# Performance work log

Hardware: AMD Instinct MI355X
Metric: run time of the kernel (lower is better)

Reference implementation:

```python
import jax, jax.numpy as jnp
import numpy as np

E, H, M = 1024, 16, 256
B, S = 2, 2048
D = E // H
SCALE = D ** -0.5


def setup_inputs() -> dict:
    key = jax.random.key(0)
    ks = jax.random.split(key, 10)
    p = 0.02
    return {
        "x": jax.random.normal(ks[0], (B, S, E), jnp.float32),
        "Wq": jax.random.normal(ks[1], (E, E), jnp.float32) * p,
        "bq": jax.random.normal(ks[2], (E,), jnp.float32) * p,
        "Wk": jax.random.normal(ks[3], (E, E), jnp.float32) * p,
        "bk": jax.random.normal(ks[4], (E,), jnp.float32) * p,
        "Wv": jax.random.normal(ks[5], (E, E), jnp.float32) * p,
        "bv": jax.random.normal(ks[6], (E,), jnp.float32) * p,
        "Wo": jax.random.normal(ks[7], (E, E), jnp.float32) * p,
        "bo": jax.random.normal(ks[8], (E,), jnp.float32) * p,
        "memory_state": jax.random.normal(ks[9], (M, E), jnp.float32) * p,
    }


def reference(x, Wq, bq, Wk, bk, Wv, bv, Wo, bo, memory_state):
    b, s, e = x.shape
    # QKV projections (torch Linear: y = x W^T + b), split heads -> [b,h,s,d]
    q = (x @ Wq.T + bq).reshape(b, s, H, D).transpose(0, 2, 1, 3)
    k = (x @ Wk.T + bk).reshape(b, s, H, D).transpose(0, 2, 1, 3)
    v = (x @ Wv.T + bv).reshape(b, s, H, D).transpose(0, 2, 1, 3)
    # full self-attention (eval mode: dropout is identity)
    attn = jax.nn.softmax(jnp.einsum("bhqd,bhkd->bhqk", q, k) * SCALE, axis=-1)
    attn_out = jnp.einsum("bhqk,bhkd->bhqd", attn, v)
    attn_out = attn_out.transpose(0, 2, 1, 3).reshape(b, s, e)
    # memory-read cross-attention on raw x against compressed memory [M,E]
    mem_w = jax.nn.softmax(jnp.einsum("bse,me->bsm", x, memory_state) * SCALE, axis=-1)
    mem_out = jnp.einsum("bsm,me->bse", mem_w, memory_state)
    out = attn_out + 0.5 * mem_out
    return out @ Wo.T + bo
```

## Files before the change

### kernel.cpp

```cpp
#include <hip/hip_runtime.h>
#include <cstdint>
#include <cstddef>


typedef __bf16 bf16;
typedef bf16  bf16x8 __attribute__((ext_vector_type(8)));
typedef bf16  bf16x4 __attribute__((ext_vector_type(4)));
typedef float f32x4  __attribute__((ext_vector_type(4)));

#define B_DIM 2
#define S_DIM 2048
#define E_DIM 1024
#define H_DIM 16
#define D_DIM 64
#define M_DIM 256
#define NROW  (B_DIM * S_DIM)
#define C1 0.18033688011112042f

__device__ __forceinline__ void async_cp16(const bf16* g, bf16* l)
{
    __builtin_amdgcn_global_load_lds(
        (const __attribute__((address_space(1))) void*)g,
        (__attribute__((address_space(3))) void*)l, 16, 0, 0);
}

__global__ void __launch_bounds__(256)
conv_all(const float* __restrict__ x,  const float* __restrict__ Wq,
         const float* __restrict__ Wk, const float* __restrict__ Wv,
         const float* __restrict__ Wo, const float* __restrict__ mem,
         bf16* __restrict__ xb,  bf16* __restrict__ Wqb,
         bf16* __restrict__ Wkb, bf16* __restrict__ Wvb,
         bf16* __restrict__ Wob, bf16* __restrict__ memb)
{
    int t = blockIdx.x * 256 + threadIdx.x;
    const float* src; bf16* dst; int off;
    if      (t <  524288) { src = x;   dst = xb;   off = t; }
    else if (t <  655360) { src = Wq;  dst = Wqb;  off = t - 524288; }
    else if (t <  786432) { src = Wk;  dst = Wkb;  off = t - 655360; }
    else if (t <  917504) { src = Wv;  dst = Wvb;  off = t - 786432; }
    else if (t < 1048576) { src = Wo;  dst = Wob;  off = t - 917504; }
    else                  { src = mem; dst = memb; off = t - 1048576; }
    const float4* p = (const float4*)src + (size_t)off * 2;
    float4 a = p[0], b = p[1];
    bf16x8 o;
    o[0] = (bf16)a.x; o[1] = (bf16)a.y; o[2] = (bf16)a.z; o[3] = (bf16)a.w;
    o[4] = (bf16)b.x; o[5] = (bf16)b.y; o[6] = (bf16)b.z; o[7] = (bf16)b.w;
    *(bf16x8*)(dst + (size_t)off * 8) = o;
}

struct GemmAcc { f32x4 a[4][4]; };

__device__ __forceinline__ void
gemm_core(const bf16* __restrict__ A, const bf16* __restrict__ Bm,
          int K, int m0, int n0, bf16* As, bf16* Bs, GemmAcc& R)
{
    const int tid  = threadIdx.x;
    const int lane = tid & 63;
    const int wave = tid >> 6;
    const int quad = lane >> 4;
    const int l16  = lane & 15;
    const int wm   = (wave >> 1) * 64;
    const int wn   = (wave & 1) * 64;

#pragma unroll
    for (int i = 0; i < 4; ++i)
#pragma unroll
        for (int j = 0; j < 4; ++j)
            R.a[i][j] = f32x4{0.f, 0.f, 0.f, 0.f};

    int s_c0  = wave * 128 + lane;
    int s_r0  = s_c0 >> 2;
    int s_k0  = (s_c0 & 3) ^ ((s_r0 >> 1) & 3);
    int s_c1  = s_c0 + 64;
    int s_r1  = s_c1 >> 2;
    int s_k1  = (s_c1 & 3) ^ ((s_r1 >> 1) & 3);
    const bf16* gA0 = A  + (size_t)(m0 + s_r0) * K + s_k0 * 8;
    const bf16* gA1 = A  + (size_t)(m0 + s_r1) * K + s_k1 * 8;
    const bf16* gB0 = Bm + (size_t)(n0 + s_r0) * K + s_k0 * 8;
    const bf16* gB1 = Bm + (size_t)(n0 + s_r1) * K + s_k1 * 8;

#define STAGE(buf, k0)                                                     \
    do {                                                                   \
        async_cp16(gA0 + (k0), &As[(buf) * 4096 + wave * 1024]);           \
        async_cp16(gA1 + (k0), &As[(buf) * 4096 + wave * 1024 + 512]);     \
        async_cp16(gB0 + (k0), &Bs[(buf) * 4096 + wave * 1024]);           \
        async_cp16(gB1 + (k0), &Bs[(buf) * 4096 + wave * 1024 + 512]);     \
    } while (0)

    STAGE(0, 0);
    int buf = 0;
    for (int k0 = 0; k0 < K; k0 += 32) {
        __syncthreads();
        if (k0 + 32 < K) STAGE(buf ^ 1, k0 + 32);

        const bf16* Ab = As + buf * 4096;
        const bf16* Bb = Bs + buf * 4096;
        bf16x8 af[4], bfr[4];
#pragma unroll
        for (int mi = 0; mi < 4; ++mi) {
            int m    = wm + mi * 16 + l16;
            int slot = quad ^ ((m >> 1) & 3);
            af[mi]   = *(const bf16x8*)(&Ab[(m * 4 + slot) * 8]);
        }
#pragma unroll
        for (int ni = 0; ni < 4; ++ni) {
            int n    = wn + ni * 16 + l16;
            int slot = quad ^ ((n >> 1) & 3);
            bfr[ni]  = *(const bf16x8*)(&Bb[(n * 4 + slot) * 8]);
        }
#pragma unroll
        for (int mi = 0; mi < 4; ++mi)
#pragma unroll
            for (int ni = 0; ni < 4; ++ni)
                R.a[mi][ni] = __builtin_amdgcn_mfma_f32_16x16x32_bf16(
                    af[mi], bfr[ni], R.a[mi][ni], 0, 0, 0);
        buf ^= 1;
    }
#undef STAGE
}

template <typename OUT_T>
__global__ void __launch_bounds__(256, 2)
gemm_nt(const bf16* __restrict__ A, const bf16* __restrict__ Bm,
        const float* __restrict__ bias, OUT_T* __restrict__ C,
        int N, int K)
{
    __shared__ __align__(16) bf16 As[2 * 4096];
    __shared__ __align__(16) bf16 Bs[2 * 4096];
    const int m0 = blockIdx.y * 128, n0 = blockIdx.x * 128;
    GemmAcc R;
    gemm_core(A, Bm, K, m0, n0, As, Bs, R);
    const int lane = threadIdx.x & 63, wave = threadIdx.x >> 6;
    const int quad = lane >> 4, l16 = lane & 15;
    const int wm = (wave >> 1) * 64, wn = (wave & 1) * 64;
#pragma unroll
    for (int ni = 0; ni < 4; ++ni) {
        int col  = n0 + wn + ni * 16 + l16;
        float bv = bias ? bias[col] : 0.f;
#pragma unroll
        for (int mi = 0; mi < 4; ++mi)
#pragma unroll
            for (int r = 0; r < 4; ++r) {
                int rowg = m0 + wm + mi * 16 + quad * 4 + r;
                C[(size_t)rowg * N + col] = (OUT_T)(R.a[mi][ni][r] + bv);
            }
    }
}

__global__ void __launch_bounds__(256, 2)
gemm_qkv(const bf16* __restrict__ A,
         const bf16* __restrict__ Wq, const bf16* __restrict__ Wk,
         const bf16* __restrict__ Wv,
         const float* __restrict__ bq, const float* __restrict__ bk,
         const float* __restrict__ bv,
         bf16* __restrict__ q, bf16* __restrict__ k, bf16* __restrict__ vt)
{
    __shared__ __align__(16) bf16 As[2 * 4096];
    __shared__ __align__(16) bf16 Bs[2 * 4096];
    const int widx = blockIdx.x >> 3;
    const int n0   = (blockIdx.x & 7) * 128;
    const int m0   = blockIdx.y * 128;
    const bf16*  Bm = (widx == 0) ? Wq : (widx == 1) ? Wk : Wv;
    const float* bi = (widx == 0) ? bq : (widx == 1) ? bk : bv;
    GemmAcc R;
    gemm_core(A, Bm, E_DIM, m0, n0, As, Bs, R);

    const int lane = threadIdx.x & 63, wave = threadIdx.x >> 6;
    const int quad = lane >> 4, l16 = lane & 15;
    const int wm = (wave >> 1) * 64, wn = (wave & 1) * 64;

    if (widx < 2) {
        bf16* C = (widx == 0) ? q : k;
        float scale = (widx == 0) ? C1 : 1.0f;
#pragma unroll
        for (int ni = 0; ni < 4; ++ni) {
            int col  = n0 + wn + ni * 16 + l16;
            float bb = bi[col];
#pragma unroll
            for (int mi = 0; mi < 4; ++mi)
#pragma unroll
                for (int r = 0; r < 4; ++r) {
                    int rowg = m0 + wm + mi * 16 + quad * 4 + r;
                    C[(size_t)rowg * E_DIM + col] =
                        (bf16)((R.a[mi][ni][r] + bb) * scale);
                }
        }
    } else {
#pragma unroll
        for (int ni = 0; ni < 4; ++ni) {
            int col = n0 + wn + ni * 16 + l16;
            float bb = bi[col];
#pragma unroll
            for (int mi = 0; mi < 4; ++mi) {
                int row0 = m0 + wm + mi * 16 + quad * 4;
                int bidx = row0 >> 11, s = row0 & 2047;
                bf16x4 pk;
#pragma unroll
                for (int r = 0; r < 4; ++r) pk[r] = (bf16)(R.a[mi][ni][r] + bb);
                *(bf16x4*)(&vt[((size_t)(bidx * H_DIM) * 64 + col) * S_DIM + s]) = pk;
            }
        }
    }
}

__global__ void __launch_bounds__(256)
transpose2d(const bf16* __restrict__ in, bf16* __restrict__ out, int R, int C)
{
    __shared__ __align__(16) bf16 t[64][72];
    const int tid = threadIdx.x;
    const int r0  = blockIdx.y * 64;
    const int c0  = blockIdx.x * 64;
#pragma unroll
    for (int i = 0; i < 2; ++i) {
        int c  = tid + i * 256;
        int rr = c >> 3, cc = c & 7;
        *(bf16x8*)(&t[rr][cc * 8]) =
            *(const bf16x8*)(&in[(size_t)(r0 + rr) * C + c0 + cc * 8]);
    }
    __syncthreads();
#pragma unroll
    for (int i = 0; i < 2; ++i) {
        int c  = tid + i * 256;
        int cr = c >> 3, sc = c & 7;
        bf16x8 val;
#pragma unroll
        for (int j = 0; j < 8; ++j) val[j] = t[sc * 8 + j][cr];
        *(bf16x8*)(&out[(size_t)(c0 + cr) * R + r0 + sc * 8]) = val;
    }
}

__global__ void __launch_bounds__(256)
softmax_mem(bf16* __restrict__ P)
{
    const int tid  = threadIdx.x;
    const int lane = tid & 63;
    const int wave = tid >> 6;
    const int row  = blockIdx.x * 4 + wave;
    bf16* lp = P + (size_t)row * M_DIM;

    bf16x4 raw = *(const bf16x4*)(lp + lane * 4);
    float t[4];
#pragma unroll
    for (int j = 0; j < 4; ++j) t[j] = (float)raw[j] * C1;

    float m = fmaxf(fmaxf(t[0], t[1]), fmaxf(t[2], t[3]));
#pragma unroll
    for (int s = 1; s < 64; s <<= 1) m = fmaxf(m, __shfl_xor(m, s));

    float p[4], sum = 0.f;
#pragma unroll
    for (int j = 0; j < 4; ++j) { p[j] = exp2f(t[j] - m); sum += p[j]; }
#pragma unroll
    for (int s = 1; s < 64; s <<= 1) sum += __shfl_xor(sum, s);

    float inv = 1.f / sum;
    bf16x4 o;
#pragma unroll
    for (int j = 0; j < 4; ++j) o[j] = (bf16)(p[j] * inv);
    *(bf16x4*)(lp + lane * 4) = o;
}

__global__ void __launch_bounds__(256, 2)
flash_attn(const bf16* __restrict__ q, const bf16* __restrict__ k,
           const bf16* __restrict__ vt, const bf16* __restrict__ memout,
           bf16* __restrict__ outc)
{
    __shared__ __align__(16) bf16 Ks[2 * 4096];
    __shared__ __align__(16) bf16 Vs[2 * 4096];
    __shared__ __align__(16) bf16 plds[4 * 32 * 72];
    const int tid  = threadIdx.x;
    const int lane = tid & 63;
    const int wave = tid >> 6;
    const int quad = lane >> 4;
    const int l16  = lane & 15;
    const int lid = blockIdx.x;
    const int h   = (lid & 7) + 8 * ((lid >> 8) & 1);
    const int qt  = (lid >> 3) & 15;
    const int b   = (lid >> 7) & 1;
    const int q0  = qt * 128 + wave * 32;

    const bf16* qb = q  + (size_t)(b * S_DIM + q0) * E_DIM + h * D_DIM;
    const bf16* kb = k  + (size_t)(b * S_DIM) * E_DIM + h * D_DIM;
    const bf16* vb = vt + (size_t)(b * H_DIM + h) * D_DIM * S_DIM;
    bf16* pw = plds + wave * 32 * 72;

    const int s_s0 = wave * 128 + lane;
    const int s_r0 = s_s0 >> 3;
    const int s_g0 = (s_s0 & 7) ^ (s_r0 & 7);
    const int s_s1 = s_s0 + 64;
    const int s_r1 = s_s1 >> 3;
    const int s_g1 = (s_s1 & 7) ^ (s_r1 & 7);
    const bf16* gK0 = kb + (size_t)s_r0 * E_DIM + s_g0 * 8;
    const bf16* gK1 = kb + (size_t)s_r1 * E_DIM + s_g1 * 8;
    const bf16* gV0 = vb + (size_t)s_r0 * S_DIM + s_g0 * 8;
    const bf16* gV1 = vb + (size_t)s_r1 * S_DIM + s_g1 * 8;

#define STAGE_KV(buf, kt)                                                   \
    do {                                                                    \
        async_cp16(gK0 + (size_t)(kt) * E_DIM, &Ks[(buf) * 4096 + wave * 1024]);       \
        async_cp16(gK1 + (size_t)(kt) * E_DIM, &Ks[(buf) * 4096 + wave * 1024 + 512]); \
        async_cp16(gV0 + (kt), &Vs[(buf) * 4096 + wave * 1024]);            \
        async_cp16(gV1 + (kt), &Vs[(buf) * 4096 + wave * 1024 + 512]);      \
    } while (0)

    bf16x8 a_q[2][2];
#pragma unroll
    for (int mf = 0; mf < 2; ++mf)
#pragma unroll
        for (int kc = 0; kc < 2; ++kc)
            a_q[mf][kc] = *(const bf16x8*)(
                qb + (size_t)(mf * 16 + l16) * E_DIM + kc * 32 + quad * 8);

    f32x4 o_acc[2][4];
#pragma unroll
    for (int mf = 0; mf < 2; ++mf)
#pragma unroll
        for (int i = 0; i < 4; ++i) o_acc[mf][i] = f32x4{0.f, 0.f, 0.f, 0.f};
    float l_part[2] = {0.f, 0.f};

    STAGE_KV(0, 0);
    int buf = 0;
    for (int kt = 0; kt < S_DIM; kt += 64) {
        __syncthreads();
        if (kt + 64 < S_DIM) STAGE_KV(buf ^ 1, kt + 64);
        const bf16* Kb = Ks + buf * 4096;
        const bf16* Vb = Vs + buf * 4096;

        f32x4 sc[2][4];
#pragma unroll
        for (int nb = 0; nb < 4; ++nb) {
            bf16x8 bk[2];
#pragma unroll
            for (int kc = 0; kc < 2; ++kc) {
                int row  = nb * 16 + l16;
                int slot = (kc * 4 + quad) ^ (row & 7);
                bk[kc]   = *(const bf16x8*)(&Kb[row * 64 + slot * 8]);
            }
#pragma unroll
            for (int mf = 0; mf < 2; ++mf) {
                f32x4 a = f32x4{0.f, 0.f, 0.f, 0.f};
                a = __builtin_amdgcn_mfma_f32_16x16x32_bf16(bk[0], a_q[mf][0], a, 0, 0, 0);
                a = __builtin_amdgcn_mfma_f32_16x16x32_bf16(bk[1], a_q[mf][1], a, 0, 0, 0);
                sc[mf][nb] = a;
            }
        }

#pragma unroll
        for (int mf = 0; mf < 2; ++mf)
#pragma unroll
            for (int nb = 0; nb < 4; ++nb) {
                bf16x4 pk;
#pragma unroll
                for (int r = 0; r < 4; ++r) {
                    float e = exp2f(sc[mf][nb][r]);
                    l_part[mf] += e;
                    pk[r] = (bf16)e;
                }
                *(bf16x4*)(&pw[(mf * 16 + l16) * 72 + nb * 16 + quad * 4]) = pk;
            }

        bf16x8 a_p[2][2];
#pragma unroll
        for (int mf = 0; mf < 2; ++mf)
#pragma unroll
            for (int kc = 0; kc < 2; ++kc)
                a_p[mf][kc] = *(const bf16x8*)(
                    &pw[(mf * 16 + l16) * 72 + kc * 32 + quad * 8]);
#pragma unroll
        for (int nd = 0; nd < 4; ++nd) {
            bf16x8 bv[2];
#pragma unroll
            for (int kc = 0; kc < 2; ++kc) {
                int row  = nd * 16 + l16;
                int slot = (kc * 4 + quad) ^ (row & 7);
                bv[kc]   = *(const bf16x8*)(&Vb[row * 64 + slot * 8]);
            }
#pragma unroll
            for (int mf = 0; mf < 2; ++mf) {
                o_acc[mf][nd] = __builtin_amdgcn_mfma_f32_16x16x32_bf16(
                    a_p[mf][0], bv[0], o_acc[mf][nd], 0, 0, 0);
                o_acc[mf][nd] = __builtin_amdgcn_mfma_f32_16x16x32_bf16(
                    a_p[mf][1], bv[1], o_acc[mf][nd], 0, 0, 0);
            }
        }
        buf ^= 1;
    }
#undef STAGE_KV

    float linv[2][4];
#pragma unroll
    for (int mf = 0; mf < 2; ++mf) {
        float L = l_part[mf];
        L += __shfl_xor(L, 16);
        L += __shfl_xor(L, 32);
        float Li = 1.f / L;
#pragma unroll
        for (int r = 0; r < 4; ++r)
            linv[mf][r] = __shfl(Li, quad * 4 + r);
    }

    bf16* ob       = outc   + (size_t)(b * S_DIM + q0) * E_DIM + h * D_DIM;
    const bf16* mb = memout + (size_t)(b * S_DIM + q0) * E_DIM + h * D_DIM;
#pragma unroll
    for (int mf = 0; mf < 2; ++mf)
#pragma unroll
        for (int nd = 0; nd < 4; ++nd)
#pragma unroll
            for (int r = 0; r < 4; ++r) {
                size_t off = (size_t)(mf * 16 + quad * 4 + r) * E_DIM + nd * 16 + l16;
                float v = o_acc[mf][nd][r] * linv[mf][r] + 0.5f * (float)mb[off];
                ob[off] = (bf16)v;
            }
}

extern "C" void kernel_launch(void* const* d_in, const int* in_sizes, int n_in,
                              void* d_out, int out_size, void* d_ws, size_t ws_size,
                              hipStream_t stream)
{
    (void)in_sizes; (void)n_in; (void)out_size; (void)ws_size;
    const float* x   = (const float*)d_in[0];
    const float* Wq  = (const float*)d_in[1];
    const float* bq  = (const float*)d_in[2];
    const float* Wk  = (const float*)d_in[3];
    const float* bk  = (const float*)d_in[4];
    const float* Wv  = (const float*)d_in[5];
    const float* bv  = (const float*)d_in[6];
    const float* Wo  = (const float*)d_in[7];
    const float* bo  = (const float*)d_in[8];
    const float* mem = (const float*)d_in[9];
    float* out = (float*)d_out;

    bf16* w = (bf16*)d_ws;
    const size_t NE = (size_t)NROW * E_DIM;
    const size_t EE = (size_t)E_DIM * E_DIM;
    bf16* xb      = w;
    bf16* q_ws    = w + NE;
    bf16* k_ws    = w + 2 * NE;
    bf16* mo_ws   = w + 3 * NE;
    bf16* Wqb     = w + 4 * NE;
    bf16* Wkb     = Wqb + EE;
    bf16* Wvb     = Wkb + EE;
    bf16* Wob     = Wvb + EE;
    bf16* memb    = Wob + EE;
    bf16* lg_ws   = memb + (size_t)M_DIM * E_DIM;
    bf16* memt_ws = lg_ws + (size_t)NROW * M_DIM;
    bf16* vt_ws = (bf16*)d_out;

    dim3 blk(256);

    conv_all<<<dim3(4224), blk, 0, stream>>>(
        x, Wq, Wk, Wv, Wo, mem, xb, Wqb, Wkb, Wvb, Wob, memb);

    transpose2d<<<dim3(E_DIM / 64, M_DIM / 64), blk, 0, stream>>>(
        memb, memt_ws, M_DIM, E_DIM);
    gemm_nt<bf16><<<dim3(M_DIM / 128, NROW / 128), blk, 0, stream>>>(
        xb, memb, nullptr, lg_ws, M_DIM, E_DIM);
    softmax_mem<<<dim3(NROW / 4), blk, 0, stream>>>(lg_ws);
    gemm_nt<bf16><<<dim3(E_DIM / 128, NROW / 128), blk, 0, stream>>>(
        lg_ws, memt_ws, nullptr, mo_ws, E_DIM, M_DIM);

    gemm_qkv<<<dim3(3 * E_DIM / 128, NROW / 128), blk, 0, stream>>>(
        xb, Wqb, Wkb, Wvb, bq, bk, bv, q_ws, k_ws, vt_ws);

    flash_attn<<<dim3(512), blk, 0, stream>>>(
        q_ws, k_ws, vt_ws, mo_ws, q_ws);

    gemm_nt<float><<<dim3(E_DIM / 128, NROW / 128), blk, 0, stream>>>(
        q_ws, Wob, bo, out, E_DIM, E_DIM);
}
```

Before: 253.3 us.

## Shrink flash-attn tiles, reuse KV LDS for P, fold mem transpose into conversion

Flash attention now gives each wave 16 query rows instead of 32 and launches twice as many blocks, with an XCD-aware mapping of (batch, head, q-tile). The dedicated P staging buffer is dropped; after a barrier, P is written into the current K/V LDS buffer, which cuts LDS use so four blocks can share a CU. The separate transpose kernel for memory_state is removed, and the transposed copy is written by the conversion kernel through scattered stores. GEMM launch bounds rise to 3 blocks per SU, which constrains registers and risks spills; the extra barrier per KV tile adds a synchronisation cost.

```diff
diff --git a/kernel.cpp b/kernel.cpp
--- a/kernel.cpp
+++ b/kernel.cpp
@@ -30,22 +30,29 @@
          const float* __restrict__ Wo, const float* __restrict__ mem,
          bf16* __restrict__ xb,  bf16* __restrict__ Wqb,
          bf16* __restrict__ Wkb, bf16* __restrict__ Wvb,
-         bf16* __restrict__ Wob, bf16* __restrict__ memb)
+         bf16* __restrict__ Wob, bf16* __restrict__ memb,
+         bf16* __restrict__ memt)
 {
     int t = blockIdx.x * 256 + threadIdx.x;
-    const float* src; bf16* dst; int off;
+    const float* src; bf16* dst; int off; bool is_mem = false;
     if      (t <  524288) { src = x;   dst = xb;   off = t; }
     else if (t <  655360) { src = Wq;  dst = Wqb;  off = t - 524288; }
     else if (t <  786432) { src = Wk;  dst = Wkb;  off = t - 655360; }
     else if (t <  917504) { src = Wv;  dst = Wvb;  off = t - 786432; }
     else if (t < 1048576) { src = Wo;  dst = Wob;  off = t - 917504; }
-    else                  { src = mem; dst = memb; off = t - 1048576; }
+    else                  { src = mem; dst = memb; off = t - 1048576; is_mem = true; }
     const float4* p = (const float4*)src + (size_t)off * 2;
     float4 a = p[0], b = p[1];
     bf16x8 o;
     o[0] = (bf16)a.x; o[1] = (bf16)a.y; o[2] = (bf16)a.z; o[3] = (bf16)a.w;
     o[4] = (bf16)b.x; o[5] = (bf16)b.y; o[6] = (bf16)b.z; o[7] = (bf16)b.w;
     *(bf16x8*)(dst + (size_t)off * 8) = o;
+    if (is_mem) {
+        int r = off >> 7, c0 = (off & 127) * 8;
+#pragma unroll
+        for (int j = 0; j < 8; ++j)
+            memt[(size_t)(c0 + j) * M_DIM + r] = o[j];
+    }
 }
 
 struct GemmAcc { f32x4 a[4][4]; };
@@ -120,7 +127,7 @@
 }
 
 template <typename OUT_T>
-__global__ void __launch_bounds__(256, 2)
+__global__ void __launch_bounds__(256, 3)
 gemm_nt(const bf16* __restrict__ A, const bf16* __restrict__ Bm,
         const float* __restrict__ bias, OUT_T* __restrict__ C,
         int N, int K)
@@ -147,7 +154,7 @@
     }
 }
 
-__global__ void __launch_bounds__(256, 2)
+__global__ void __launch_bounds__(256, 3)
 gemm_qkv(const bf16* __restrict__ A,
          const bf16* __restrict__ Wq, const bf16* __restrict__ Wk,
          const bf16* __restrict__ Wv,
@@ -204,32 +211,6 @@
 }
 
 __global__ void __launch_bounds__(256)
-transpose2d(const bf16* __restrict__ in, bf16* __restrict__ out, int R, int C)
-{
-    __shared__ __align__(16) bf16 t[64][72];
-    const int tid = threadIdx.x;
-    const int r0  = blockIdx.y * 64;
-    const int c0  = blockIdx.x * 64;
-#pragma unroll
-    for (int i = 0; i < 2; ++i) {
-        int c  = tid + i * 256;
-        int rr = c >> 3, cc = c & 7;
-        *(bf16x8*)(&t[rr][cc * 8]) =
-            *(const bf16x8*)(&in[(size_t)(r0 + rr) * C + c0 + cc * 8]);
-    }
-    __syncthreads();
-#pragma unroll
-    for (int i = 0; i < 2; ++i) {
-        int c  = tid + i * 256;
-        int cr = c >> 3, sc = c & 7;
-        bf16x8 val;
-#pragma unroll
-        for (int j = 0; j < 8; ++j) val[j] = t[sc * 8 + j][cr];
-        *(bf16x8*)(&out[(size_t)(c0 + cr) * R + r0 + sc * 8]) = val;
-    }
-}
-
-__global__ void __launch_bounds__(256)
 softmax_mem(bf16* __restrict__ P)
 {
     const int tid  = threadIdx.x;
@@ -260,29 +241,30 @@
     *(bf16x4*)(lp + lane * 4) = o;
 }
 
-__global__ void __launch_bounds__(256, 2)
+__global__ void __launch_bounds__(256, 4)
 flash_attn(const bf16* __restrict__ q, const bf16* __restrict__ k,
            const bf16* __restrict__ vt, const bf16* __restrict__ memout,
            bf16* __restrict__ outc)
 {
     __shared__ __align__(16) bf16 Ks[2 * 4096];
     __shared__ __align__(16) bf16 Vs[2 * 4096];
-    __shared__ __align__(16) bf16 plds[4 * 32 * 72];
     const int tid  = threadIdx.x;
     const int lane = tid & 63;
     const int wave = tid >> 6;
     const int quad = lane >> 4;
     const int l16  = lane & 15;
     const int lid = blockIdx.x;
-    const int h   = (lid & 7) + 8 * ((lid >> 8) & 1);
-    const int qt  = (lid >> 3) & 15;
-    const int b   = (lid >> 7) & 1;
-    const int q0  = qt * 128 + wave * 32;
+    const int xcd = lid & 7;
+    const int kk  = lid >> 3;
+    const int qt  = kk & 31;
+    const int p   = ((kk >> 5) << 3) | xcd;
+    const int b   = p >> 4;
+    const int h   = p & 15;
+    const int q0  = qt * 64 + wave * 16;
 
     const bf16* qb = q  + (size_t)(b * S_DIM + q0) * E_DIM + h * D_DIM;
     const bf16* kb = k  + (size_t)(b * S_DIM) * E_DIM + h * D_DIM;
     const bf16* vb = vt + (size_t)(b * H_DIM + h) * D_DIM * S_DIM;
-    bf16* pw = plds + wave * 32 * 72;
 
     const int s_s0 = wave * 128 + lane;
     const int s_r0 = s_s0 >> 3;
@@ -303,20 +285,15 @@
         async_cp16(gV1 + (kt), &Vs[(buf) * 4096 + wave * 1024 + 512]);      \
     } while (0)
 
-    bf16x8 a_q[2][2];
-#pragma unroll
-    for (int mf = 0; mf < 2; ++mf)
-#pragma unroll
-        for (int kc = 0; kc < 2; ++kc)
-            a_q[mf][kc] = *(const bf16x8*)(
-                qb + (size_t)(mf * 16 + l16) * E_DIM + kc * 32 + quad * 8);
-
-    f32x4 o_acc[2][4];
-#pragma unroll
-    for (int mf = 0; mf < 2; ++mf)
-#pragma unroll
-        for (int i = 0; i < 4; ++i) o_acc[mf][i] = f32x4{0.f, 0.f, 0.f, 0.f};
-    float l_part[2] = {0.f, 0.f};
+    bf16x8 a_q[2];
+#pragma unroll
+    for (int kc = 0; kc < 2; ++kc)
+        a_q[kc] = *(const bf16x8*)(qb + (size_t)l16 * E_DIM + kc * 32 + quad * 8);
+
+    f32x4 o_acc[4];
+#pragma unroll
+    for (int i = 0; i < 4; ++i) o_acc[i] = f32x4{0.f, 0.f, 0.f, 0.f};
+    float l_part = 0.f;
 
     STAGE_KV(0, 0);
     int buf = 0;
@@ -326,91 +303,86 @@
         const bf16* Kb = Ks + buf * 4096;
         const bf16* Vb = Vs + buf * 4096;
 
-        f32x4 sc[2][4];
+        f32x4 sc[4];
 #pragma unroll
         for (int nb = 0; nb < 4; ++nb) {
-            bf16x8 bk[2];
-#pragma unroll
-            for (int kc = 0; kc < 2; ++kc) {
-                int row  = nb * 16 + l16;
-                int slot = (kc * 4 + quad) ^ (row & 7);
-                bk[kc]   = *(const bf16x8*)(&Kb[row * 64 + slot * 8]);
+            bf16x8 bk0, bk1;
+            {
+                int row = nb * 16 + l16;
+                int sl0 = (0 * 4 + quad) ^ (row & 7);
+                int sl1 = (1 * 4 + quad) ^ (row & 7);
+                bk0 = *(const bf16x8*)(&Kb[row * 64 + sl0 * 8]);
+                bk1 = *(const bf16x8*)(&Kb[row * 64 + sl1 * 8]);
             }
-#pragma unroll
-            for (int mf = 0; mf < 2; ++mf) {
-                f32x4 a = f32x4{0.f, 0.f, 0.f, 0.f};
-                a = __builtin_amdgcn_mfma_f32_16x16x32_bf16(bk[0], a_q[mf][0], a, 0, 0, 0);
-                a = __builtin_amdgcn_mfma_f32_16x16x32_bf16(bk[1], a_q[mf][1], a, 0, 0, 0);
-                sc[mf][nb] = a;
-            }
-        }
-
-#pragma unroll
-        for (int mf = 0; mf < 2; ++mf)
-#pragma unroll
-            for (int nb = 0; nb < 4; ++nb) {
-                bf16x4 pk;
-#pragma unroll
-                for (int r = 0; r < 4; ++r) {
-                    float e = exp2f(sc[mf][nb][r]);
-                    l_part[mf] += e;
-                    pk[r] = (bf16)e;
-                }
-                *(bf16x4*)(&pw[(mf * 16 + l16) * 72 + nb * 16 + quad * 4]) = pk;
-            }
-
-        bf16x8 a_p[2][2];
-#pragma unroll
-        for (int mf = 0; mf < 2; ++mf)
-#pragma unroll
-            for (int kc = 0; kc < 2; ++kc)
-                a_p[mf][kc] = *(const bf16x8*)(
-                    &pw[(mf * 16 + l16) * 72 + kc * 32 + quad * 8]);
-#pragma unroll
-        for (int nd = 0; nd < 4; ++nd) {
-            bf16x8 bv[2];
+            f32x4 a = f32x4{0.f, 0.f, 0.f, 0.f};
+            a = __builtin_amdgcn_mfma_f32_16x16x32_bf16(bk0, a_q[0], a, 0, 0, 0);
+            a = __builtin_amdgcn_mfma_f32_16x16x32_bf16(bk1, a_q[1], a, 0, 0, 0);
+            sc[nb] = a;
+        }
+
+        bf16x8 bv[4][2];
+#pragma unroll
+        for (int nd = 0; nd < 4; ++nd)
 #pragma unroll
             for (int kc = 0; kc < 2; ++kc) {
                 int row  = nd * 16 + l16;
                 int slot = (kc * 4 + quad) ^ (row & 7);
-                bv[kc]   = *(const bf16x8*)(&Vb[row * 64 + slot * 8]);
+                bv[nd][kc] = *(const bf16x8*)(&Vb[row * 64 + slot * 8]);
             }
-#pragma unroll
-            for (int mf = 0; mf < 2; ++mf) {
-                o_acc[mf][nd] = __builtin_amdgcn_mfma_f32_16x16x32_bf16(
-                    a_p[mf][0], bv[0], o_acc[mf][nd], 0, 0, 0);
-                o_acc[mf][nd] = __builtin_amdgcn_mfma_f32_16x16x32_bf16(
-                    a_p[mf][1], bv[1], o_acc[mf][nd], 0, 0, 0);
+
+        asm volatile("s_waitcnt lgkmcnt(0)\n\ts_barrier" ::: "memory");
+
+        bf16* pw = ((wave < 2) ? Ks : Vs) + buf * 4096 + (wave & 1) * 2048;
+#pragma unroll
+        for (int nb = 0; nb < 4; ++nb) {
+            bf16x4 pk;
+#pragma unroll
+            for (int r = 0; r < 4; ++r) {
+                float e = exp2f(sc[nb][r]);
+                l_part += e;
+                pk[r] = (bf16)e;
             }
+            int slot = ((nb * 2 + (quad >> 1)) ^ (l16 & 7));
+            *(bf16x4*)(&pw[l16 * 64 + slot * 8 + (quad & 1) * 4]) = pk;
+        }
+
+        bf16x8 a_p[2];
+#pragma unroll
+        for (int kc = 0; kc < 2; ++kc) {
+            int slot = (kc * 4 + quad) ^ (l16 & 7);
+            a_p[kc]  = *(const bf16x8*)(&pw[l16 * 64 + slot * 8]);
+        }
+
+#pragma unroll
+        for (int nd = 0; nd < 4; ++nd) {
+            o_acc[nd] = __builtin_amdgcn_mfma_f32_16x16x32_bf16(
+                a_p[0], bv[nd][0], o_acc[nd], 0, 0, 0);
+            o_acc[nd] = __builtin_amdgcn_mfma_f32_16x16x32_bf16(
+                a_p[1], bv[nd][1], o_acc[nd], 0, 0, 0);
         }
         buf ^= 1;
     }
 #undef STAGE_KV
 
-    float linv[2][4];
-#pragma unroll
-    for (int mf = 0; mf < 2; ++mf) {
-        float L = l_part[mf];
-        L += __shfl_xor(L, 16);
-        L += __shfl_xor(L, 32);
-        float Li = 1.f / L;
-#pragma unroll
-        for (int r = 0; r < 4; ++r)
-            linv[mf][r] = __shfl(Li, quad * 4 + r);
-    }
+    float L = l_part;
+    L += __shfl_xor(L, 16);
+    L += __shfl_xor(L, 32);
+    float Li = 1.f / L;
+    float linv[4];
+#pragma unroll
+    for (int r = 0; r < 4; ++r)
+        linv[r] = __shfl(Li, quad * 4 + r);
 
     bf16* ob       = outc   + (size_t)(b * S_DIM + q0) * E_DIM + h * D_DIM;
     const bf16* mb = memout + (size_t)(b * S_DIM + q0) * E_DIM + h * D_DIM;
 #pragma unroll
-    for (int mf = 0; mf < 2; ++mf)
-#pragma unroll
-        for (int nd = 0; nd < 4; ++nd)
-#pragma unroll
-            for (int r = 0; r < 4; ++r) {
-                size_t off = (size_t)(mf * 16 + quad * 4 + r) * E_DIM + nd * 16 + l16;
-                float v = o_acc[mf][nd][r] * linv[mf][r] + 0.5f * (float)mb[off];
-                ob[off] = (bf16)v;
-            }
+    for (int nd = 0; nd < 4; ++nd)
+#pragma unroll
+        for (int r = 0; r < 4; ++r) {
+            size_t off = (size_t)(quad * 4 + r) * E_DIM + nd * 16 + l16;
+            float v = o_acc[nd][r] * linv[r] + 0.5f * (float)mb[off];
+            ob[off] = (bf16)v;
+        }
 }
 
 extern "C" void kernel_launch(void* const* d_in, const int* in_sizes, int n_in,
@@ -449,10 +421,8 @@
     dim3 blk(256);
 
     conv_all<<<dim3(4224), blk, 0, stream>>>(
-        x, Wq, Wk, Wv, Wo, mem, xb, Wqb, Wkb, Wvb, Wob, memb);
-
-    transpose2d<<<dim3(E_DIM / 64, M_DIM / 64), blk, 0, stream>>>(
-        memb, memt_ws, M_DIM, E_DIM);
+        x, Wq, Wk, Wv, Wo, mem, xb, Wqb, Wkb, Wvb, Wob, memb, memt_ws);
+
     gemm_nt<bf16><<<dim3(M_DIM / 128, NROW / 128), blk, 0, stream>>>(
         xb, memb, nullptr, lg_ws, M_DIM, E_DIM);
     softmax_mem<<<dim3(NROW / 4), blk, 0, stream>>>(lg_ws);
@@ -462,7 +432,7 @@
     gemm_qkv<<<dim3(3 * E_DIM / 128, NROW / 128), blk, 0, stream>>>(
         xb, Wqb, Wkb, Wvb, bq, bk, bv, q_ws, k_ws, vt_ws);
 
-    flash_attn<<<dim3(512), blk, 0, stream>>>(
+    flash_attn<<<dim3(1024), blk, 0, stream>>>(
         q_ws, k_ws, vt_ws, mo_ws, q_ws);
 
     gemm_nt<float><<<dim3(E_DIM / 128, NROW / 128), blk, 0, stream>>>(
```

Measured after the change: 251.4 us. Within noise of the previous version (-0.7%).

## Fuse memory-logit GEMM into QKV kernel and memory-output GEMM into flash attention

Applied to the files above, without the earlier changes.

The x·memᵀ logits GEMM now runs as extra column blocks of the QKV projection kernel. The P·mem GEMM moves into the flash-attention epilogue, which reads a 0.5-prescaled transposed memory produced by the conversion kernel, so the standalone transpose and the mem_out round trip are gone. Flash attention also reuses the K/V LDS buffers for the P tile after a barrier, prefetches V fragments earlier, and remaps blocks to XCDs. GEMM occupancy hints rise to 3 blocks per CU. The trade-offs are an extra barrier per KV tile, more register pressure, and scattered 2-byte transposed writes in conv_all.

```diff
diff --git a/kernel.cpp b/kernel.cpp
--- a/kernel.cpp
+++ b/kernel.cpp
@@ -30,22 +30,30 @@
          const float* __restrict__ Wo, const float* __restrict__ mem,
          bf16* __restrict__ xb,  bf16* __restrict__ Wqb,
          bf16* __restrict__ Wkb, bf16* __restrict__ Wvb,
-         bf16* __restrict__ Wob, bf16* __restrict__ memb)
+         bf16* __restrict__ Wob, bf16* __restrict__ memb,
+         bf16* __restrict__ memt)
 {
     int t = blockIdx.x * 256 + threadIdx.x;
-    const float* src; bf16* dst; int off;
+    const float* src; bf16* dst; int off; bool is_mem = false;
     if      (t <  524288) { src = x;   dst = xb;   off = t; }
     else if (t <  655360) { src = Wq;  dst = Wqb;  off = t - 524288; }
     else if (t <  786432) { src = Wk;  dst = Wkb;  off = t - 655360; }
     else if (t <  917504) { src = Wv;  dst = Wvb;  off = t - 786432; }
     else if (t < 1048576) { src = Wo;  dst = Wob;  off = t - 917504; }
-    else                  { src = mem; dst = memb; off = t - 1048576; }
+    else                  { src = mem; dst = memb; off = t - 1048576; is_mem = true; }
     const float4* p = (const float4*)src + (size_t)off * 2;
     float4 a = p[0], b = p[1];
     bf16x8 o;
     o[0] = (bf16)a.x; o[1] = (bf16)a.y; o[2] = (bf16)a.z; o[3] = (bf16)a.w;
     o[4] = (bf16)b.x; o[5] = (bf16)b.y; o[6] = (bf16)b.z; o[7] = (bf16)b.w;
     *(bf16x8*)(dst + (size_t)off * 8) = o;
+    if (is_mem) {
+        int r = off >> 7, c0 = (off & 127) * 8;
+        float h[8] = {a.x, a.y, a.z, a.w, b.x, b.y, b.z, b.w};
+#pragma unroll
+        for (int j = 0; j < 8; ++j)
+            memt[(size_t)(c0 + j) * M_DIM + r] = (bf16)(0.5f * h[j]);
+    }
 }
 
 struct GemmAcc { f32x4 a[4][4]; };
@@ -120,7 +128,7 @@
 }
 
 template <typename OUT_T>
-__global__ void __launch_bounds__(256, 2)
+__global__ void __launch_bounds__(256, 3)
 gemm_nt(const bf16* __restrict__ A, const bf16* __restrict__ Bm,
         const float* __restrict__ bias, OUT_T* __restrict__ C,
         int N, int K)
@@ -147,21 +155,23 @@
     }
 }
 
-__global__ void __launch_bounds__(256, 2)
-gemm_qkv(const bf16* __restrict__ A,
-         const bf16* __restrict__ Wq, const bf16* __restrict__ Wk,
-         const bf16* __restrict__ Wv,
-         const float* __restrict__ bq, const float* __restrict__ bk,
-         const float* __restrict__ bv,
-         bf16* __restrict__ q, bf16* __restrict__ k, bf16* __restrict__ vt)
+__global__ void __launch_bounds__(256, 3)
+gemm_qkvl(const bf16* __restrict__ A,
+          const bf16* __restrict__ Wq, const bf16* __restrict__ Wk,
+          const bf16* __restrict__ Wv, const bf16* __restrict__ memb,
+          const float* __restrict__ bq, const float* __restrict__ bk,
+          const float* __restrict__ bv,
+          bf16* __restrict__ q, bf16* __restrict__ k,
+          bf16* __restrict__ vt, bf16* __restrict__ lg)
 {
     __shared__ __align__(16) bf16 As[2 * 4096];
     __shared__ __align__(16) bf16 Bs[2 * 4096];
-    const int widx = blockIdx.x >> 3;
-    const int n0   = (blockIdx.x & 7) * 128;
+    const int x    = blockIdx.x;
+    const int widx = (x < 24) ? (x >> 3) : 3;
+    const int n0   = (x < 24) ? (x & 7) * 128 : (x - 24) * 128;
     const int m0   = blockIdx.y * 128;
-    const bf16*  Bm = (widx == 0) ? Wq : (widx == 1) ? Wk : Wv;
-    const float* bi = (widx == 0) ? bq : (widx == 1) ? bk : bv;
+    const bf16*  Bm = (widx == 0) ? Wq : (widx == 1) ? Wk :
+                      (widx == 2) ? Wv : memb;
     GemmAcc R;
     gemm_core(A, Bm, E_DIM, m0, n0, As, Bs, R);
 
@@ -169,8 +179,9 @@
     const int quad = lane >> 4, l16 = lane & 15;
     const int wm = (wave >> 1) * 64, wn = (wave & 1) * 64;
 
-    if (widx < 2) {
+    if (widx == 0 || widx == 1) {
         bf16* C = (widx == 0) ? q : k;
+        const float* bi = (widx == 0) ? bq : bk;
         float scale = (widx == 0) ? C1 : 1.0f;
 #pragma unroll
         for (int ni = 0; ni < 4; ++ni) {
@@ -185,11 +196,11 @@
                         (bf16)((R.a[mi][ni][r] + bb) * scale);
                 }
         }
-    } else {
+    } else if (widx == 2) {
 #pragma unroll
         for (int ni = 0; ni < 4; ++ni) {
             int col = n0 + wn + ni * 16 + l16;
-            float bb = bi[col];
+            float bb = bv[col];
 #pragma unroll
             for (int mi = 0; mi < 4; ++mi) {
                 int row0 = m0 + wm + mi * 16 + quad * 4;
@@ -200,32 +211,18 @@
                 *(bf16x4*)(&vt[((size_t)(bidx * H_DIM) * 64 + col) * S_DIM + s]) = pk;
             }
         }
-    }
-}
-
-__global__ void __launch_bounds__(256)
-transpose2d(const bf16* __restrict__ in, bf16* __restrict__ out, int R, int C)
-{
-    __shared__ __align__(16) bf16 t[64][72];
-    const int tid = threadIdx.x;
-    const int r0  = blockIdx.y * 64;
-    const int c0  = blockIdx.x * 64;
-#pragma unroll
-    for (int i = 0; i < 2; ++i) {
-        int c  = tid + i * 256;
-        int rr = c >> 3, cc = c & 7;
-        *(bf16x8*)(&t[rr][cc * 8]) =
-            *(const bf16x8*)(&in[(size_t)(r0 + rr) * C + c0 + cc * 8]);
-    }
-    __syncthreads();
-#pragma unroll
-    for (int i = 0; i < 2; ++i) {
-        int c  = tid + i * 256;
-        int cr = c >> 3, sc = c & 7;
-        bf16x8 val;
-#pragma unroll
-        for (int j = 0; j < 8; ++j) val[j] = t[sc * 8 + j][cr];
-        *(bf16x8*)(&out[(size_t)(c0 + cr) * R + r0 + sc * 8]) = val;
+    } else {
+#pragma unroll
+        for (int ni = 0; ni < 4; ++ni) {
+            int col = n0 + wn + ni * 16 + l16;
+#pragma unroll
+            for (int mi = 0; mi < 4; ++mi)
+#pragma unroll
+                for (int r = 0; r < 4; ++r) {
+                    int rowg = m0 + wm + mi * 16 + quad * 4 + r;
+                    lg[(size_t)rowg * M_DIM + col] = (bf16)R.a[mi][ni][r];
+                }
+        }
     }
 }
 
@@ -262,27 +259,28 @@
 
 __global__ void __launch_bounds__(256, 2)
 flash_attn(const bf16* __restrict__ q, const bf16* __restrict__ k,
-           const bf16* __restrict__ vt, const bf16* __restrict__ memout,
-           bf16* __restrict__ outc)
+           const bf16* __restrict__ vt, const bf16* __restrict__ Pmem,
+           const bf16* __restrict__ memt, bf16* __restrict__ outc)
 {
     __shared__ __align__(16) bf16 Ks[2 * 4096];
     __shared__ __align__(16) bf16 Vs[2 * 4096];
-    __shared__ __align__(16) bf16 plds[4 * 32 * 72];
     const int tid  = threadIdx.x;
     const int lane = tid & 63;
     const int wave = tid >> 6;
     const int quad = lane >> 4;
     const int l16  = lane & 15;
     const int lid = blockIdx.x;
-    const int h   = (lid & 7) + 8 * ((lid >> 8) & 1);
-    const int qt  = (lid >> 3) & 15;
-    const int b   = (lid >> 7) & 1;
+    const int xcd = lid & 7;
+    const int kk  = lid >> 3;
+    const int qt  = kk & 15;
+    const int p   = ((kk >> 4) << 3) | xcd;
+    const int b   = p >> 4;
+    const int h   = p & 15;
     const int q0  = qt * 128 + wave * 32;
 
     const bf16* qb = q  + (size_t)(b * S_DIM + q0) * E_DIM + h * D_DIM;
     const bf16* kb = k  + (size_t)(b * S_DIM) * E_DIM + h * D_DIM;
     const bf16* vb = vt + (size_t)(b * H_DIM + h) * D_DIM * S_DIM;
-    bf16* pw = plds + wave * 32 * 72;
 
     const int s_s0 = wave * 128 + lane;
     const int s_r0 = s_s0 >> 3;
@@ -329,22 +327,36 @@
         f32x4 sc[2][4];
 #pragma unroll
         for (int nb = 0; nb < 4; ++nb) {
-            bf16x8 bk[2];
-#pragma unroll
-            for (int kc = 0; kc < 2; ++kc) {
-                int row  = nb * 16 + l16;
-                int slot = (kc * 4 + quad) ^ (row & 7);
-                bk[kc]   = *(const bf16x8*)(&Kb[row * 64 + slot * 8]);
+            bf16x8 bk0, bk1;
+            {
+                int row = nb * 16 + l16;
+                int sl0 = quad ^ (row & 7);
+                int sl1 = (4 + quad) ^ (row & 7);
+                bk0 = *(const bf16x8*)(&Kb[row * 64 + sl0 * 8]);
+                bk1 = *(const bf16x8*)(&Kb[row * 64 + sl1 * 8]);
             }
 #pragma unroll
             for (int mf = 0; mf < 2; ++mf) {
                 f32x4 a = f32x4{0.f, 0.f, 0.f, 0.f};
-                a = __builtin_amdgcn_mfma_f32_16x16x32_bf16(bk[0], a_q[mf][0], a, 0, 0, 0);
-                a = __builtin_amdgcn_mfma_f32_16x16x32_bf16(bk[1], a_q[mf][1], a, 0, 0, 0);
+                a = __builtin_amdgcn_mfma_f32_16x16x32_bf16(bk0, a_q[mf][0], a, 0, 0, 0);
+                a = __builtin_amdgcn_mfma_f32_16x16x32_bf16(bk1, a_q[mf][1], a, 0, 0, 0);
                 sc[mf][nb] = a;
             }
         }
 
+        bf16x8 bv[4][2];
+#pragma unroll
+        for (int nd = 0; nd < 4; ++nd)
+#pragma unroll
+            for (int kc = 0; kc < 2; ++kc) {
+                int row  = nd * 16 + l16;
+                int slot = (kc * 4 + quad) ^ (row & 7);
+                bv[nd][kc] = *(const bf16x8*)(&Vb[row * 64 + slot * 8]);
+            }
+
+        asm volatile("s_waitcnt lgkmcnt(0)\n\ts_barrier" ::: "memory");
+
+        bf16* pw = ((wave < 2) ? Ks : Vs) + buf * 4096 + (wave & 1) * 2048;
 #pragma unroll
         for (int mf = 0; mf < 2; ++mf)
 #pragma unroll
@@ -356,33 +368,28 @@
                     l_part[mf] += e;
                     pk[r] = (bf16)e;
                 }
-                *(bf16x4*)(&pw[(mf * 16 + l16) * 72 + nb * 16 + quad * 4]) = pk;
+                int slot = (nb * 2 + (quad >> 1)) ^ (l16 & 7);
+                *(bf16x4*)(&pw[(mf * 16 + l16) * 64 + slot * 8 + (quad & 1) * 4]) = pk;
             }
 
         bf16x8 a_p[2][2];
 #pragma unroll
         for (int mf = 0; mf < 2; ++mf)
 #pragma unroll
-            for (int kc = 0; kc < 2; ++kc)
-                a_p[mf][kc] = *(const bf16x8*)(
-                    &pw[(mf * 16 + l16) * 72 + kc * 32 + quad * 8]);
-#pragma unroll
-        for (int nd = 0; nd < 4; ++nd) {
-            bf16x8 bv[2];
-#pragma unroll
             for (int kc = 0; kc < 2; ++kc) {
-                int row  = nd * 16 + l16;
-                int slot = (kc * 4 + quad) ^ (row & 7);
-                bv[kc]   = *(const bf16x8*)(&Vb[row * 64 + slot * 8]);
-            }
+                int slot = (kc * 4 + quad) ^ (l16 & 7);
+                a_p[mf][kc] = *(const bf16x8*)(&pw[(mf * 16 + l16) * 64 + slot * 8]);
+            }
+
+#pragma unroll
+        for (int nd = 0; nd < 4; ++nd)
 #pragma unroll
             for (int mf = 0; mf < 2; ++mf) {
                 o_acc[mf][nd] = __builtin_amdgcn_mfma_f32_16x16x32_bf16(
-                    a_p[mf][0], bv[0], o_acc[mf][nd], 0, 0, 0);
+                    a_p[mf][0], bv[nd][0], o_acc[mf][nd], 0, 0, 0);
                 o_acc[mf][nd] = __builtin_amdgcn_mfma_f32_16x16x32_bf16(
-                    a_p[mf][1], bv[1], o_acc[mf][nd], 0, 0, 0);
-            }
-        }
+                    a_p[mf][1], bv[nd][1], o_acc[mf][nd], 0, 0, 0);
+            }
         buf ^= 1;
     }
 #undef STAGE_KV
@@ -399,8 +406,32 @@
             linv[mf][r] = __shfl(Li, quad * 4 + r);
     }
 
-    bf16* ob       = outc   + (size_t)(b * S_DIM + q0) * E_DIM + h * D_DIM;
-    const bf16* mb = memout + (size_t)(b * S_DIM + q0) * E_DIM + h * D_DIM;
+    f32x4 macc[2][4];
+#pragma unroll
+    for (int mf = 0; mf < 2; ++mf)
+#pragma unroll
+        for (int i = 0; i < 4; ++i) macc[mf][i] = f32x4{0.f, 0.f, 0.f, 0.f};
+    const bf16* Pr = Pmem + (size_t)(b * S_DIM + q0) * M_DIM;
+    const bf16* Mt = memt + (size_t)(h * D_DIM) * M_DIM;
+#pragma unroll
+    for (int kc = 0; kc < 8; ++kc) {
+        bf16x8 ap[2];
+#pragma unroll
+        for (int mf = 0; mf < 2; ++mf)
+            ap[mf] = *(const bf16x8*)(
+                Pr + (size_t)(mf * 16 + l16) * M_DIM + kc * 32 + quad * 8);
+#pragma unroll
+        for (int nd = 0; nd < 4; ++nd) {
+            bf16x8 bm = *(const bf16x8*)(
+                Mt + (size_t)(nd * 16 + l16) * M_DIM + kc * 32 + quad * 8);
+#pragma unroll
+            for (int mf = 0; mf < 2; ++mf)
+                macc[mf][nd] = __builtin_amdgcn_mfma_f32_16x16x32_bf16(
+                    ap[mf], bm, macc[mf][nd], 0, 0, 0);
+        }
+    }
+
+    bf16* ob = outc + (size_t)(b * S_DIM + q0) * E_DIM + h * D_DIM;
 #pragma unroll
     for (int mf = 0; mf < 2; ++mf)
 #pragma unroll
@@ -408,8 +439,7 @@
 #pragma unroll
             for (int r = 0; r < 4; ++r) {
                 size_t off = (size_t)(mf * 16 + quad * 4 + r) * E_DIM + nd * 16 + l16;
-                float v = o_acc[mf][nd][r] * linv[mf][r] + 0.5f * (float)mb[off];
-                ob[off] = (bf16)v;
+                ob[off] = (bf16)(o_acc[mf][nd][r] * linv[mf][r] + macc[mf][nd][r]);
             }
 }
 
@@ -436,8 +466,7 @@
     bf16* xb      = w;
     bf16* q_ws    = w + NE;
     bf16* k_ws    = w + 2 * NE;
-    bf16* mo_ws   = w + 3 * NE;
-    bf16* Wqb     = w + 4 * NE;
+    bf16* Wqb     = w + 3 * NE;
     bf16* Wkb     = Wqb + EE;
     bf16* Wvb     = Wkb + EE;
     bf16* Wob     = Wvb + EE;
@@ -449,21 +478,15 @@
     dim3 blk(256);
 
     conv_all<<<dim3(4224), blk, 0, stream>>>(
-        x, Wq, Wk, Wv, Wo, mem, xb, Wqb, Wkb, Wvb, Wob, memb);
-
-    transpose2d<<<dim3(E_DIM / 64, M_DIM / 64), blk, 0, stream>>>(
-        memb, memt_ws, M_DIM, E_DIM);
-    gemm_nt<bf16><<<dim3(M_DIM / 128, NROW / 128), blk, 0, stream>>>(
-        xb, memb, nullptr, lg_ws, M_DIM, E_DIM);
+        x, Wq, Wk, Wv, Wo, mem, xb, Wqb, Wkb, Wvb, Wob, memb, memt_ws);
+
+    gemm_qkvl<<<dim3(26, NROW / 128), blk, 0, stream>>>(
+        xb, Wqb, Wkb, Wvb, memb, bq, bk, bv, q_ws, k_ws, vt_ws, lg_ws);
+
     softmax_mem<<<dim3(NROW / 4), blk, 0, stream>>>(lg_ws);
-    gemm_nt<bf16><<<dim3(E_DIM / 128, NROW / 128), blk, 0, stream>>>(
-        lg_ws, memt_ws, nullptr, mo_ws, E_DIM, M_DIM);
-
-    gemm_qkv<<<dim3(3 * E_DIM / 128, NROW / 128), blk, 0, stream>>>(
-        xb, Wqb, Wkb, Wvb, bq, bk, bv, q_ws, k_ws, vt_ws);
 
     flash_attn<<<dim3(512), blk, 0, stream>>>(
-        q_ws, k_ws, vt_ws, mo_ws, q_ws);
+        q_ws, k_ws, vt_ws, lg_ws, memt_ws, q_ws);
 
     gemm_nt<float><<<dim3(E_DIM / 128, NROW / 128), blk, 0, stream>>>(
         q_ws, Wob, bo, out, E_DIM, E_DIM);
```

Result: faster. 247.7 us (-2.2%).
